# Kernel optimization log

Hardware: AMD Instinct MI355X
Metric: run time of the kernel (lower is better)

## Reference

```python
import jax, jax.numpy as jnp
import numpy as np

N_ATOMS = 65536
N_BONDS = 131072
N_MOLS = 512
D_IN = 16
D = 128
REPEAT = 3


def _dense(key, fan_in, fan_out):
    kw, kb = jax.random.split(key)
    scale = 1.0 / np.sqrt(fan_in)
    W = jax.random.normal(kw, (fan_in, fan_out), dtype=jnp.float32) * scale
    b = jnp.zeros((fan_out,), dtype=jnp.float32)
    return W, b


def setup_inputs() -> dict:
    key = jax.random.key(0)
    ks = jax.random.split(key, 12)
    atoms = jax.random.normal(ks[0], (N_ATOMS, D_IN), dtype=jnp.float32)
    bond_orders = jax.random.uniform(ks[1], (N_BONDS,), dtype=jnp.float32)
    bond_src = jax.random.randint(ks[2], (N_BONDS,), 0, N_ATOMS, dtype=jnp.int32)
    bond_dst = jax.random.randint(ks[3], (N_BONDS,), 0, N_ATOMS, dtype=jnp.int32)
    atom_mol = jnp.sort(jax.random.randint(ks[4], (N_ATOMS,), 0, N_MOLS, dtype=jnp.int32))
    bond_mol = jnp.sort(jax.random.randint(ks[5], (N_BONDS,), 0, N_MOLS, dtype=jnp.int32))
    W_fe, b_fe = _dense(ks[6], 1, D)      # f_e : bond order -> h_e
    W_fv, b_fv = _dense(ks[7], D_IN, D)   # f_v : atom feats -> h_v
    W_fu, b_fu = _dense(ks[8], D, D)      # f_u : per-mol init from aggregated nodes
    W_e, b_e = _dense(ks[9], 5 * D, D)    # phi_e(h_e, h_e0, h_left, h_right, u)
    W_v, b_v = _dense(ks[10], 4 * D, D)   # phi_v(h_v, h_v0, e_bar_i, u)
    W_u, b_u = _dense(ks[11], 4 * D, D)   # phi_u(h_u, h_u0, e_bar, v_bar)
    return dict(atoms=atoms, bond_orders=bond_orders, W_fe=W_fe, b_fe=b_fe,
                W_fv=W_fv, b_fv=b_fv, W_fu=W_fu, b_fu=b_fu, W_e=W_e, b_e=b_e,
                W_v=W_v, b_v=b_v, W_u=W_u, b_u=b_u,
                bond_src=bond_src, bond_dst=bond_dst,
                atom_mol=atom_mol, bond_mol=bond_mol)


def reference(atoms, bond_orders, W_fe, b_fe, W_fv, b_fv, W_fu, b_fu,
              W_e, b_e, W_v, b_v, W_u, b_u,
              bond_src, bond_dst, atom_mol, bond_mol):
    seg = lambda x, ids, n: jax.ops.segment_sum(x, ids, num_segments=n)
    relu = jax.nn.relu

    # f_e / f_v / f_u initial embeddings
    h_e0 = relu(bond_orders[:, None] @ W_fe + b_fe)           # [E, D]
    h_v0 = relu(atoms @ W_fv + b_fv)                          # [N, D]
    h_u0 = relu(seg(h_v0, atom_mol, N_MOLS) @ W_fu + b_fu)    # [M, D]

    h_e, h_v, h_u = h_e0, h_v0, h_u0
    for _ in range(REPEAT):
        # phi_e(e_k, e_k_0, v_rk, v_sk, u): gather endpoints and per-bond global
        h_left = h_v[bond_src]                                # [E, D]
        h_right = h_v[bond_dst]                               # [E, D]
        u_e = h_u[bond_mol]                                   # [E, D]
        h_e = relu(jnp.concatenate([h_e, h_e0, h_left, h_right, u_e], axis=1) @ W_e + b_e)
        # rho_e_v: sum of updated edges incident to each atom (one-hot mask == scatter-add)
        e_bar_i = seg(h_e, bond_src, N_ATOMS) + seg(h_e, bond_dst, N_ATOMS)  # [N, D]
        # phi_v(v_i, v_i_0, e_bar_i, u)
        h_v = relu(jnp.concatenate([h_v, h_v0, e_bar_i, h_u[atom_mol]], axis=1) @ W_v + b_v)
        # rho_e_u / rho_v_u: per-molecule segment sums
        e_bar = seg(h_e, bond_mol, N_MOLS)                    # [M, D]
        v_bar = seg(h_v, atom_mol, N_MOLS)                    # [M, D]
        # phi_u(u, u_0, e_bar, v_bar)
        h_u = relu(jnp.concatenate([h_u, h_u0, e_bar, v_bar], axis=1) @ W_u + b_u)
    return h_u
```

## Files before the change

kernel.cpp:

```cpp
#include <hip/hip_runtime.h>
#include <hip/hip_bf16.h>
#include <stdint.h>

#define N_ATOMS 65536
#define N_BONDS 131072
#define N_MOLS  512
#define D_IN    16
#define DD      128
#define REPEAT  3
#define PITCH   136

typedef __attribute__((ext_vector_type(8))) short s8b;
typedef __attribute__((ext_vector_type(4))) float f32x4;

__device__ __forceinline__ float us2f(unsigned short s) {
    unsigned int u = ((unsigned int)s) << 16;
    float f; __builtin_memcpy(&f, &u, 4); return f;
}
__device__ __forceinline__ unsigned short f2us(float f) {
    __hip_bfloat16 h = __float2bfloat16(f);
    unsigned short s; __builtin_memcpy(&s, &h, 2); return s;
}
__device__ __forceinline__ void acc8(float* a, uint4 v) {
    unsigned short w[8]; __builtin_memcpy(w, &v, 16);
#pragma unroll
    for (int j = 0; j < 8; j++) a[j] += us2f(w[j]);
}


__global__ void k_pack_w(const float* __restrict__ W, unsigned short* __restrict__ Wpk, int K) {
    int idx = blockIdx.x * 256 + threadIdx.x;
    if (idx >= K * 128) return;
    int k = idx >> 7, n = idx & 127;
    int c = k >> 7, ks = (k >> 5) & 3, quad = (k >> 3) & 3, j = k & 7;
    int pidx = (((c * 4 + ks) * 4 + quad) * 128 + n) * 8 + j;
    Wpk[pidx] = f2us(W[k * 128 + n]);
}

__global__ void k_deg(const int* __restrict__ bsrc, const int* __restrict__ bdst,
                      int* __restrict__ deg) {
    int e = blockIdx.x * 256 + threadIdx.x;
    atomicAdd(&deg[bsrc[e]], 1);
    atomicAdd(&deg[bdst[e]], 1);
}

__global__ void k_scan1(const int* __restrict__ deg, int* __restrict__ bsum) {
    __shared__ int red[256];
    int t = threadIdx.x;
    red[t] = deg[blockIdx.x * 256 + t];
    __syncthreads();
    for (int s = 128; s > 0; s >>= 1) {
        if (t < s) red[t] += red[t + s];
        __syncthreads();
    }
    if (t == 0) bsum[blockIdx.x] = red[0];
}

__global__ void k_scan2(const int* __restrict__ bsum, int* __restrict__ boff) {
    __shared__ int s[256];
    int t = threadIdx.x;
    s[t] = bsum[t];
    __syncthreads();
    if (t == 0) {
        int run = 0;
        for (int i = 0; i < 256; i++) { int v = s[i]; s[i] = run; run += v; }
    }
    __syncthreads();
    boff[t] = s[t];
}

__global__ void k_scan3(const int* __restrict__ deg, const int* __restrict__ boff,
                        int* __restrict__ rowptr, int* __restrict__ cursor) {
    __shared__ int s[256];
    int t = threadIdx.x;
    int i = blockIdx.x * 256 + t;
    int d = deg[i];
    s[t] = d;
    __syncthreads();
    for (int off = 1; off < 256; off <<= 1) {
        int v = (t >= off) ? s[t - off] : 0;
        __syncthreads();
        s[t] += v;
        __syncthreads();
    }
    int val = boff[blockIdx.x] + s[t] - d;
    rowptr[i] = val;
    cursor[i] = val;
    if (i == N_ATOMS - 1) rowptr[N_ATOMS] = val + d;
}

__global__ void k_fill(const int* __restrict__ bsrc, const int* __restrict__ bdst,
                       int* __restrict__ cursor, int* __restrict__ adj) {
    int e = blockIdx.x * 256 + threadIdx.x;
    int p = atomicAdd(&cursor[bsrc[e]], 1); adj[p] = e;
    int q = atomicAdd(&cursor[bdst[e]], 1); adj[q] = e;
}

__global__ void k_molptr2(const int* __restrict__ bmol, const int* __restrict__ amol,
                          int* __restrict__ bptr, int* __restrict__ aptr) {
    int m = threadIdx.x;
    if (m > N_MOLS) return;
    const int* ids = blockIdx.x ? amol : bmol;
    int rows = blockIdx.x ? N_ATOMS : N_BONDS;
    int* out = blockIdx.x ? aptr : bptr;
    int lo = 0, hi = rows;
    while (lo < hi) {
        int mid = (lo + hi) >> 1;
        if (ids[mid] < m) lo = mid + 1; else hi = mid;
    }
    out[m] = lo;
}


__global__ __launch_bounds__(256) void k_molsum_s(const unsigned short* __restrict__ x,
                                                  const int* __restrict__ mptr,
                                                  float* __restrict__ out, int S) {
    __shared__ float red[16 * 128];
    int m = blockIdx.x / S, s = blockIdx.x - m * S;
    int b = mptr[m], e = mptr[m + 1];
    int len = (e - b + S - 1) / S;
    int r0 = b + s * len;
    int r1 = min(r0 + len, e);
    int rl = threadIdx.x >> 4, g = threadIdx.x & 15;
    float acc[8] = {0,0,0,0,0,0,0,0};
    for (int r = r0 + rl; r < r1; r += 16)
        acc8(acc, *reinterpret_cast<const uint4*>(x + (size_t)r * DD + g * 8));
#pragma unroll
    for (int j = 0; j < 8; j++) red[rl * 128 + g * 8 + j] = acc[j];
    __syncthreads();
    if (threadIdx.x < 128) {
        int col = threadIdx.x;
        float sum = 0.f;
#pragma unroll
        for (int i = 0; i < 16; i++) sum += red[i * 128 + col];
        atomicAdd(&out[(size_t)m * DD + col], sum);
    }
}

__global__ void k_mol_init(const float* __restrict__ ns, const float* __restrict__ Wfu,
                           const float* __restrict__ bfu, float* __restrict__ hu0) {
    int idx = blockIdx.x * 256 + threadIdx.x;
    int m = idx >> 7, d = idx & 127;
    float acc = bfu[d];
    for (int k = 0; k < DD; k++)
        acc = fmaf(ns[m*DD + k], Wfu[k*DD + d], acc);
    hu0[idx] = fmaxf(acc, 0.f);
}

__global__ void k_yrow2(const float* __restrict__ hu,
                        const float* __restrict__ We, const float* __restrict__ be,
                        const float* __restrict__ Wv, const float* __restrict__ bv,
                        float* __restrict__ yue, float* __restrict__ yuv,
                        float* __restrict__ ebar, float* __restrict__ vbar) {
    int idx = blockIdx.x * 256 + threadIdx.x;
    if (idx < N_MOLS * DD) ebar[idx] = 0.f;
    else                   vbar[idx - N_MOLS * DD] = 0.f;
    int half = idx >= N_MOLS * DD;
    int md = half ? idx - N_MOLS * DD : idx;
    int m = md >> 7, d = md & 127;
    const float* W  = half ? Wv + 384 * DD : We + 512 * DD;
    float acc = half ? bv[d] : be[d];
    for (int k = 0; k < DD; k++)
        acc = fmaf(hu[m*DD + k], W[k*DD + d], acc);
    (half ? yuv : yue)[md] = acc;
}

__global__ __launch_bounds__(256) void k_ye0(
        const float* __restrict__ bo, const float* __restrict__ Wfe,
        const float* __restrict__ bfe, const unsigned short* __restrict__ Wpk,
        unsigned short* __restrict__ he, unsigned short* __restrict__ ye0) {
    __shared__ __align__(16) unsigned short xs[128 * PITCH];
    __shared__ float sbo[128];
    int tid = threadIdx.x;
    int e0 = blockIdx.x * 128;
    if (tid < 128) sbo[tid] = bo[e0 + tid];
    int wv = tid >> 6, lane = tid & 63, quad = lane >> 4, l15 = lane & 15;
    f32x4 acc[8][2];
#pragma unroll
    for (int mt = 0; mt < 8; mt++) {
        acc[mt][0] = (f32x4){0.f,0.f,0.f,0.f};
        acc[mt][1] = (f32x4){0.f,0.f,0.f,0.f};
    }
    __syncthreads();
    for (int t = 0; t < 8; t++) {
        int u = tid + t * 256;
        int i = u >> 4, g = (u & 15) * 8;
        float b = sbo[i];
        unsigned short tmp[8];
#pragma unroll
        for (int j = 0; j < 8; j++)
            tmp[j] = f2us(fmaxf(fmaf(b, Wfe[g + j], bfe[g + j]), 0.f));
        uint4 val; __builtin_memcpy(&val, tmp, 16);
        *reinterpret_cast<uint4*>(&xs[i * PITCH + g]) = val;
        *reinterpret_cast<uint4*>(he + (size_t)(e0 + i) * DD + g) = val;
    }
    __syncthreads();
#pragma unroll
    for (int ks = 0; ks < 4; ks++) {
        const unsigned short* wb = Wpk + ((1 * 4 + ks) * 4 + quad) * 1024 + (wv * 32 + l15) * 8;
        s8b b0 = *reinterpret_cast<const s8b*>(wb);
        s8b b1 = *reinterpret_cast<const s8b*>(wb + 128);
#pragma unroll
        for (int mt = 0; mt < 8; mt++) {
            s8b afr = *reinterpret_cast<const s8b*>(&xs[(mt*16 + l15) * PITCH + ks*32 + quad*8]);
            acc[mt][0] = __builtin_amdgcn_mfma_f32_16x16x32_bf16(afr, b0, acc[mt][0], 0, 0, 0);
            acc[mt][1] = __builtin_amdgcn_mfma_f32_16x16x32_bf16(afr, b1, acc[mt][1], 0, 0, 0);
        }
    }
#pragma unroll
    for (int mt = 0; mt < 8; mt++)
#pragma unroll
        for (int r = 0; r < 4; r++) {
            int row = e0 + mt*16 + quad*4 + r;
#pragma unroll
            for (int nt = 0; nt < 2; nt++) {
                int col = wv*32 + nt*16 + l15;
                ye0[(size_t)row * DD + col] = f2us(acc[mt][nt][r]);
            }
        }
}

__global__ __launch_bounds__(256) void k_nodes_f(
        const float* __restrict__ atoms, const float* __restrict__ Wfv,
        const float* __restrict__ bfv, const unsigned short* __restrict__ Wpk,
        unsigned short* __restrict__ hv, unsigned short* __restrict__ yv0,
        float* __restrict__ node_sum) {
    __shared__ __align__(16) unsigned short xs[128 * PITCH];
    int tid = threadIdx.x;
    int gid = blockIdx.x * 256 + tid;
    if (gid < N_MOLS * DD) node_sum[gid] = 0.f;
    int n0 = blockIdx.x * 128;
    int wv = tid >> 6, lane = tid & 63, quad = lane >> 4, l15 = lane & 15;
    f32x4 acc[8][2];
#pragma unroll
    for (int mt = 0; mt < 8; mt++) {
        acc[mt][0] = (f32x4){0.f,0.f,0.f,0.f};
        acc[mt][1] = (f32x4){0.f,0.f,0.f,0.f};
    }
    for (int t = 0; t < 8; t++) {
        int u = tid + t * 256;
        int i = u >> 4, g = (u & 15) * 8;
        int row = n0 + i;
        float a[D_IN];
#pragma unroll
        for (int k = 0; k < D_IN; k++) a[k] = atoms[(size_t)row * D_IN + k];
        unsigned short tmp[8];
#pragma unroll
        for (int j = 0; j < 8; j++) {
            float acc1 = bfv[g + j];
#pragma unroll
            for (int k = 0; k < D_IN; k++)
                acc1 = fmaf(a[k], Wfv[k*DD + g + j], acc1);
            tmp[j] = f2us(fmaxf(acc1, 0.f));
        }
        uint4 val; __builtin_memcpy(&val, tmp, 16);
        *reinterpret_cast<uint4*>(&xs[i * PITCH + g]) = val;
        *reinterpret_cast<uint4*>(hv + (size_t)row * DD + g) = val;
    }
    __syncthreads();
#pragma unroll
    for (int ks = 0; ks < 4; ks++) {
        const unsigned short* wb = Wpk + ((1 * 4 + ks) * 4 + quad) * 1024 + (wv * 32 + l15) * 8;
        s8b b0 = *reinterpret_cast<const s8b*>(wb);
        s8b b1 = *reinterpret_cast<const s8b*>(wb + 128);
#pragma unroll
        for (int mt = 0; mt < 8; mt++) {
            s8b afr = *reinterpret_cast<const s8b*>(&xs[(mt*16 + l15) * PITCH + ks*32 + quad*8]);
            acc[mt][0] = __builtin_amdgcn_mfma_f32_16x16x32_bf16(afr, b0, acc[mt][0], 0, 0, 0);
            acc[mt][1] = __builtin_amdgcn_mfma_f32_16x16x32_bf16(afr, b1, acc[mt][1], 0, 0, 0);
        }
    }
#pragma unroll
    for (int mt = 0; mt < 8; mt++)
#pragma unroll
        for (int r = 0; r < 4; r++) {
            int row = n0 + mt*16 + quad*4 + r;
#pragma unroll
            for (int nt = 0; nt < 2; nt++) {
                int col = wv*32 + nt*16 + l15;
                yv0[(size_t)row * DD + col] = f2us(acc[mt][nt][r]);
            }
        }
}

__global__ __launch_bounds__(256) void k_zsd(
        const unsigned short* __restrict__ hv, const unsigned short* __restrict__ Wpk,
        unsigned short* __restrict__ Zs, unsigned short* __restrict__ Zd) {
    __shared__ __align__(16) unsigned short xs[128 * PITCH];
    int tid = threadIdx.x;
    int n0 = blockIdx.x * 128;
    int wv = tid >> 6, lane = tid & 63, quad = lane >> 4, l15 = lane & 15;
    f32x4 aS[8][2], aD[8][2];
#pragma unroll
    for (int mt = 0; mt < 8; mt++) {
        aS[mt][0] = (f32x4){0.f,0.f,0.f,0.f}; aS[mt][1] = (f32x4){0.f,0.f,0.f,0.f};
        aD[mt][0] = (f32x4){0.f,0.f,0.f,0.f}; aD[mt][1] = (f32x4){0.f,0.f,0.f,0.f};
    }
    for (int t = 0; t < 8; t++) {
        int u = tid + t * 256;
        int i = u >> 4, g = (u & 15) * 8;
        *reinterpret_cast<uint4*>(&xs[i * PITCH + g]) =
            *reinterpret_cast<const uint4*>(hv + (size_t)(n0 + i) * DD + g);
    }
    __syncthreads();
#pragma unroll
    for (int ks = 0; ks < 4; ks++) {
        const unsigned short* wbS = Wpk + ((2 * 4 + ks) * 4 + quad) * 1024 + (wv * 32 + l15) * 8;
        const unsigned short* wbD = Wpk + ((3 * 4 + ks) * 4 + quad) * 1024 + (wv * 32 + l15) * 8;
        s8b s0 = *reinterpret_cast<const s8b*>(wbS);
        s8b s1 = *reinterpret_cast<const s8b*>(wbS + 128);
        s8b d0 = *reinterpret_cast<const s8b*>(wbD);
        s8b d1 = *reinterpret_cast<const s8b*>(wbD + 128);
#pragma unroll
        for (int mt = 0; mt < 8; mt++) {
            s8b afr = *reinterpret_cast<const s8b*>(&xs[(mt*16 + l15) * PITCH + ks*32 + quad*8]);
            aS[mt][0] = __builtin_amdgcn_mfma_f32_16x16x32_bf16(afr, s0, aS[mt][0], 0, 0, 0);
            aS[mt][1] = __builtin_amdgcn_mfma_f32_16x16x32_bf16(afr, s1, aS[mt][1], 0, 0, 0);
            aD[mt][0] = __builtin_amdgcn_mfma_f32_16x16x32_bf16(afr, d0, aD[mt][0], 0, 0, 0);
            aD[mt][1] = __builtin_amdgcn_mfma_f32_16x16x32_bf16(afr, d1, aD[mt][1], 0, 0, 0);
        }
    }
#pragma unroll
    for (int mt = 0; mt < 8; mt++)
#pragma unroll
        for (int r = 0; r < 4; r++) {
            int row = n0 + mt*16 + quad*4 + r;
#pragma unroll
            for (int nt = 0; nt < 2; nt++) {
                int col = wv*32 + nt*16 + l15;
                Zs[(size_t)row * DD + col] = f2us(aS[mt][nt][r]);
                Zd[(size_t)row * DD + col] = f2us(aD[mt][nt][r]);
            }
        }
}

__global__ __launch_bounds__(256) void k_phi_e(
        unsigned short* __restrict__ he, const unsigned short* __restrict__ ye0,
        const unsigned short* __restrict__ Zs, const unsigned short* __restrict__ Zd,
        const unsigned short* __restrict__ Wpk, const float* __restrict__ yue,
        const int* __restrict__ bsrc, const int* __restrict__ bdst,
        const int* __restrict__ bmol) {
    __shared__ __align__(16) unsigned short xs[128 * PITCH];
    __shared__ int ssrc[128], sdst[128], smol[128];
    int tid = threadIdx.x;
    int e0 = blockIdx.x * 128;
    if (tid < 128) {
        ssrc[tid] = bsrc[e0 + tid];
        sdst[tid] = bdst[e0 + tid];
        smol[tid] = bmol[e0 + tid];
    }
    int wv = tid >> 6, lane = tid & 63, quad = lane >> 4, l15 = lane & 15;
    f32x4 acc[8][2];
#pragma unroll
    for (int mt = 0; mt < 8; mt++) {
        acc[mt][0] = (f32x4){0.f,0.f,0.f,0.f};
        acc[mt][1] = (f32x4){0.f,0.f,0.f,0.f};
    }
    for (int t = 0; t < 8; t++) {
        int u = tid + t * 256;
        int i = u >> 4, g = (u & 15) * 8;
        *reinterpret_cast<uint4*>(&xs[i * PITCH + g]) =
            *reinterpret_cast<const uint4*>(he + (size_t)(e0 + i) * DD + g);
    }
    __syncthreads();
#pragma unroll
    for (int ks = 0; ks < 4; ks++) {
        const unsigned short* wb = Wpk + ((0 * 4 + ks) * 4 + quad) * 1024 + (wv * 32 + l15) * 8;
        s8b b0 = *reinterpret_cast<const s8b*>(wb);
        s8b b1 = *reinterpret_cast<const s8b*>(wb + 128);
#pragma unroll
        for (int mt = 0; mt < 8; mt++) {
            s8b afr = *reinterpret_cast<const s8b*>(&xs[(mt*16 + l15) * PITCH + ks*32 + quad*8]);
            acc[mt][0] = __builtin_amdgcn_mfma_f32_16x16x32_bf16(afr, b0, acc[mt][0], 0, 0, 0);
            acc[mt][1] = __builtin_amdgcn_mfma_f32_16x16x32_bf16(afr, b1, acc[mt][1], 0, 0, 0);
        }
    }
    __syncthreads();
    for (int t = 0; t < 8; t++) {
        int u = tid + t * 256;
        int i = u >> 4, g = (u & 15) * 8;
        float s[8] = {0,0,0,0,0,0,0,0};
        acc8(s, *reinterpret_cast<const uint4*>(ye0 + (size_t)(e0 + i) * DD + g));
        acc8(s, *reinterpret_cast<const uint4*>(Zs  + (size_t)ssrc[i] * DD + g));
        acc8(s, *reinterpret_cast<const uint4*>(Zd  + (size_t)sdst[i] * DD + g));
        const float* yr = yue + (size_t)smol[i] * DD + g;
        float4 y0 = *reinterpret_cast<const float4*>(yr);
        float4 y1 = *reinterpret_cast<const float4*>(yr + 4);
        s[0] += y0.x; s[1] += y0.y; s[2] += y0.z; s[3] += y0.w;
        s[4] += y1.x; s[5] += y1.y; s[6] += y1.z; s[7] += y1.w;
        unsigned short tmp[8];
#pragma unroll
        for (int j = 0; j < 8; j++) tmp[j] = f2us(s[j]);
        uint4 val; __builtin_memcpy(&val, tmp, 16);
        *reinterpret_cast<uint4*>(&xs[i * PITCH + g]) = val;
    }
    __syncthreads();
#pragma unroll
    for (int mt = 0; mt < 8; mt++)
#pragma unroll
        for (int r = 0; r < 4; r++) {
            int rl = mt*16 + quad*4 + r;
#pragma unroll
            for (int nt = 0; nt < 2; nt++) {
                int col = wv*32 + nt*16 + l15;
                float v = acc[mt][nt][r] + us2f(xs[rl * PITCH + col]);
                he[(size_t)(e0 + rl) * DD + col] = f2us(fmaxf(v, 0.f));
            }
        }
}

__global__ __launch_bounds__(256) void k_ebar(const unsigned short* __restrict__ he,
                                              const int* __restrict__ rowptr,
                                              const int* __restrict__ adj,
                                              unsigned short* __restrict__ ebar_i) {
    int n = blockIdx.x * 16 + (threadIdx.x >> 4);
    int g = threadIdx.x & 15;
    int b = rowptr[n], e = rowptr[n + 1];
    float acc[8] = {0,0,0,0,0,0,0,0};
    int j = b;
    for (; j + 3 < e; j += 4) {
        uint4 v0 = *reinterpret_cast<const uint4*>(he + (size_t)adj[j]     * DD + g * 8);
        uint4 v1 = *reinterpret_cast<const uint4*>(he + (size_t)adj[j + 1] * DD + g * 8);
        uint4 v2 = *reinterpret_cast<const uint4*>(he + (size_t)adj[j + 2] * DD + g * 8);
        uint4 v3 = *reinterpret_cast<const uint4*>(he + (size_t)adj[j + 3] * DD + g * 8);
        acc8(acc, v0); acc8(acc, v1); acc8(acc, v2); acc8(acc, v3);
    }
    for (; j < e; j++)
        acc8(acc, *reinterpret_cast<const uint4*>(he + (size_t)adj[j] * DD + g * 8));
    unsigned short o[8];
#pragma unroll
    for (int k = 0; k < 8; k++) o[k] = f2us(acc[k]);
    uint4 ov; __builtin_memcpy(&ov, o, 16);
    *reinterpret_cast<uint4*>(ebar_i + (size_t)n * DD + g * 8) = ov;
}

__global__ __launch_bounds__(256) void k_phi_v(
        unsigned short* __restrict__ hv, const unsigned short* __restrict__ ebar_i,
        const unsigned short* __restrict__ yv0,
        const unsigned short* __restrict__ Wpk, const float* __restrict__ yuv,
        const int* __restrict__ amol) {
    __shared__ __align__(16) unsigned short xs[128 * PITCH];
    __shared__ int smol[128];
    int tid = threadIdx.x;
    int n0 = blockIdx.x * 128;
    if (tid < 128) smol[tid] = amol[n0 + tid];
    int wv = tid >> 6, lane = tid & 63, quad = lane >> 4, l15 = lane & 15;
    f32x4 acc[8][2];
#pragma unroll
    for (int mt = 0; mt < 8; mt++) {
        acc[mt][0] = (f32x4){0.f,0.f,0.f,0.f};
        acc[mt][1] = (f32x4){0.f,0.f,0.f,0.f};
    }
    const unsigned short* bases[2] = { hv + (size_t)n0 * DD, ebar_i + (size_t)n0 * DD };
    const int wcs[2] = {0, 2};
    for (int c = 0; c < 2; c++) {
        if (c) __syncthreads();
        for (int t = 0; t < 8; t++) {
            int u = tid + t * 256;
            int i = u >> 4, g = (u & 15) * 8;
            *reinterpret_cast<uint4*>(&xs[i * PITCH + g]) =
                *reinterpret_cast<const uint4*>(bases[c] + (size_t)i * DD + g);
        }
        __syncthreads();
        int WC = wcs[c];
#pragma unroll
        for (int ks = 0; ks < 4; ks++) {
            const unsigned short* wb = Wpk + ((WC * 4 + ks) * 4 + quad) * 1024 + (wv * 32 + l15) * 8;
            s8b b0 = *reinterpret_cast<const s8b*>(wb);
            s8b b1 = *reinterpret_cast<const s8b*>(wb + 128);
#pragma unroll
            for (int mt = 0; mt < 8; mt++) {
                s8b afr = *reinterpret_cast<const s8b*>(&xs[(mt*16 + l15) * PITCH + ks*32 + quad*8]);
                acc[mt][0] = __builtin_amdgcn_mfma_f32_16x16x32_bf16(afr, b0, acc[mt][0], 0, 0, 0);
                acc[mt][1] = __builtin_amdgcn_mfma_f32_16x16x32_bf16(afr, b1, acc[mt][1], 0, 0, 0);
            }
        }
    }
    __syncthreads();
    for (int t = 0; t < 8; t++) {
        int u = tid + t * 256;
        int i = u >> 4, g = (u & 15) * 8;
        float s[8] = {0,0,0,0,0,0,0,0};
        acc8(s, *reinterpret_cast<const uint4*>(yv0 + (size_t)(n0 + i) * DD + g));
        const float* yr = yuv + (size_t)smol[i] * DD + g;
        float4 y0 = *reinterpret_cast<const float4*>(yr);
        float4 y1 = *reinterpret_cast<const float4*>(yr + 4);
        s[0] += y0.x; s[1] += y0.y; s[2] += y0.z; s[3] += y0.w;
        s[4] += y1.x; s[5] += y1.y; s[6] += y1.z; s[7] += y1.w;
        unsigned short tmp[8];
#pragma unroll
        for (int j = 0; j < 8; j++) tmp[j] = f2us(s[j]);
        uint4 val; __builtin_memcpy(&val, tmp, 16);
        *reinterpret_cast<uint4*>(&xs[i * PITCH + g]) = val;
    }
    __syncthreads();
#pragma unroll
    for (int mt = 0; mt < 8; mt++)
#pragma unroll
        for (int r = 0; r < 4; r++) {
            int rl = mt*16 + quad*4 + r;
#pragma unroll
            for (int nt = 0; nt < 2; nt++) {
                int col = wv*32 + nt*16 + l15;
                float v = acc[mt][nt][r] + us2f(xs[rl * PITCH + col]);
                hv[(size_t)(n0 + rl) * DD + col] = f2us(fmaxf(v, 0.f));
            }
        }
}

__global__ void k_phi_u(const float* __restrict__ hu_in, const float* __restrict__ hu0,
                        const float* __restrict__ ebar, const float* __restrict__ vbar,
                        const float* __restrict__ Wu, const float* __restrict__ bu,
                        float* __restrict__ hu_out, float* __restrict__ dout) {
    int idx = blockIdx.x * 256 + threadIdx.x;
    int m = idx >> 7, d = idx & 127;
    float acc = bu[d];
    const float* segs[4] = { hu_in + m*DD, hu0 + m*DD, ebar + m*DD, vbar + m*DD };
    for (int s = 0; s < 4; s++) {
        const float* x = segs[s];
        const float* W = Wu + (s*DD)*DD + d;
        for (int k = 0; k < DD; k++)
            acc = fmaf(x[k], W[k*DD], acc);
    }
    float v = fmaxf(acc, 0.f);
    hu_out[idx] = v;
    dout[idx] = v;
}


extern "C" void kernel_launch(void* const* d_in, const int* in_sizes, int n_in,
                              void* d_out, int out_size, void* d_ws, size_t ws_size,
                              hipStream_t stream) {
    const float* atoms = (const float*)d_in[0];
    const float* bo    = (const float*)d_in[1];
    const float* Wfe   = (const float*)d_in[2];
    const float* bfe   = (const float*)d_in[3];
    const float* Wfv   = (const float*)d_in[4];
    const float* bfv   = (const float*)d_in[5];
    const float* Wfu   = (const float*)d_in[6];
    const float* bfu   = (const float*)d_in[7];
    const float* We    = (const float*)d_in[8];
    const float* be    = (const float*)d_in[9];
    const float* Wv    = (const float*)d_in[10];
    const float* bv    = (const float*)d_in[11];
    const float* Wu    = (const float*)d_in[12];
    const float* bu    = (const float*)d_in[13];
    const int* bsrc    = (const int*)d_in[14];
    const int* bdst    = (const int*)d_in[15];
    const int* amol    = (const int*)d_in[16];
    const int* bmol    = (const int*)d_in[17];

    char* p = (char*)d_ws;
    auto alloc = [&](size_t bytes) {
        char* r = p;
        p += (bytes + 255) & ~(size_t)255;
        return r;
    };
    unsigned short* he     = (unsigned short*)alloc((size_t)N_BONDS * DD * 2);
    unsigned short* ye0    = (unsigned short*)alloc((size_t)N_BONDS * DD * 2);
    unsigned short* hv     = (unsigned short*)alloc((size_t)N_ATOMS * DD * 2);
    unsigned short* yv0    = (unsigned short*)alloc((size_t)N_ATOMS * DD * 2);
    unsigned short* Zs     = (unsigned short*)alloc((size_t)N_ATOMS * DD * 2);
    unsigned short* Zd     = (unsigned short*)alloc((size_t)N_ATOMS * DD * 2);
    unsigned short* ebar_i = (unsigned short*)alloc((size_t)N_ATOMS * DD * 2);
    unsigned short* WeP    = (unsigned short*)alloc((size_t)640 * DD * 2);
    unsigned short* WvP    = (unsigned short*)alloc((size_t)512 * DD * 2);
    int* deg      = (int*)alloc((size_t)N_ATOMS * 4);
    int* rowptr   = (int*)alloc((size_t)(N_ATOMS + 1) * 4);
    int* cursor   = (int*)alloc((size_t)N_ATOMS * 4);
    int* adj      = (int*)alloc((size_t)2 * N_BONDS * 4);
    int* bmol_ptr = (int*)alloc((size_t)(N_MOLS + 1) * 4);
    int* amol_ptr = (int*)alloc((size_t)(N_MOLS + 1) * 4);
    int* bsum     = (int*)alloc((size_t)256 * 4);
    int* boff     = (int*)alloc((size_t)256 * 4);
    float* node_sum = (float*)alloc((size_t)N_MOLS * DD * 4);
    float* hu0   = (float*)alloc((size_t)N_MOLS * DD * 4);
    float* huA   = (float*)alloc((size_t)N_MOLS * DD * 4);
    float* huB   = (float*)alloc((size_t)N_MOLS * DD * 4);
    float* ebar  = (float*)alloc((size_t)N_MOLS * DD * 4);
    float* vbar  = (float*)alloc((size_t)N_MOLS * DD * 4);
    float* yue   = (float*)alloc((size_t)N_MOLS * DD * 4);
    float* yuv   = (float*)alloc((size_t)N_MOLS * DD * 4);

    hipMemsetAsync(deg, 0, (size_t)N_ATOMS * 4, stream);
    k_deg<<<N_BONDS/256, 256, 0, stream>>>(bsrc, bdst, deg);
    k_scan1<<<256, 256, 0, stream>>>(deg, bsum);
    k_scan2<<<1, 256, 0, stream>>>(bsum, boff);
    k_scan3<<<256, 256, 0, stream>>>(deg, boff, rowptr, cursor);
    k_fill<<<N_BONDS/256, 256, 0, stream>>>(bsrc, bdst, cursor, adj);
    k_molptr2<<<2, 1024, 0, stream>>>(bmol, amol, bmol_ptr, amol_ptr);

    k_pack_w<<<(640*DD)/256, 256, 0, stream>>>(We, WeP, 640);
    k_pack_w<<<(512*DD)/256, 256, 0, stream>>>(Wv, WvP, 512);

    k_ye0<<<N_BONDS/128, 256, 0, stream>>>(bo, Wfe, bfe, WeP, he, ye0);
    k_nodes_f<<<N_ATOMS/128, 256, 0, stream>>>(atoms, Wfv, bfv, WvP, hv, yv0, node_sum);
    k_molsum_s<<<N_MOLS*2, 256, 0, stream>>>(hv, amol_ptr, node_sum, 2);
    k_mol_init<<<(N_MOLS*DD)/256, 256, 0, stream>>>(node_sum, Wfu, bfu, hu0);

    const float* hu_in = hu0; float* hu_out = huA;

    for (int r = 0; r < REPEAT; r++) {
        k_yrow2<<<(2*N_MOLS*DD)/256, 256, 0, stream>>>(hu_in, We, be, Wv, bv,
                                                       yue, yuv, ebar, vbar);
        k_zsd<<<N_ATOMS/128, 256, 0, stream>>>(hv, WeP, Zs, Zd);
        k_phi_e<<<N_BONDS/128, 256, 0, stream>>>(he, ye0, Zs, Zd, WeP, yue,
                                                 bsrc, bdst, bmol);
        k_ebar<<<N_ATOMS/16, 256, 0, stream>>>(he, rowptr, adj, ebar_i);
        k_molsum_s<<<N_MOLS*4, 256, 0, stream>>>(he, bmol_ptr, ebar, 4);
        k_phi_v<<<N_ATOMS/128, 256, 0, stream>>>(hv, ebar_i, yv0, WvP, yuv, amol);
        k_molsum_s<<<N_MOLS*2, 256, 0, stream>>>(hv, amol_ptr, vbar, 2);
        k_phi_u<<<(N_MOLS*DD)/256, 256, 0, stream>>>(hu_in, hu0, ebar, vbar, Wu, bu,
                                                     hu_out, (float*)d_out);

        hu_in = hu_out; hu_out = (hu_out == huA) ? huB : huA;
    }
}
```

Before: 523.2 us.

## Fuse per-molecule sums and edge gathers into GEMM epilogues, cut kernel launches

The per-molecule sums of edge and node features now happen inside the phi_e and phi_v epilogues. Each thread keeps a running sum over consecutive rows of the same molecule and flushes it with an atomicAdd, which replaces the separate k_molsum_s passes. The incident-edge gather (e_bar_i) moves into phi_v, so the ebar_i intermediate buffer and the k_ebar launch go away. The u-projection rows (yue/yuv) are computed in the mol_init and phi_u kernels, buffer zeroing moves into k_zsd, and the scan and weight-pack kernels are merged. This removes launches and extra global traffic, at the cost of more atomic contention and an irregular gather inside phi_v that may lower its occupancy.

```diff
diff --git a/kernel.cpp b/kernel.cpp
--- a/kernel.cpp
+++ b/kernel.cpp
@@ -28,13 +28,17 @@
 }
 
 
-__global__ void k_pack_w(const float* __restrict__ W, unsigned short* __restrict__ Wpk, int K) {
-    int idx = blockIdx.x * 256 + threadIdx.x;
-    if (idx >= K * 128) return;
+__device__ __forceinline__ void pack_one(const float* W, unsigned short* Wpk, int idx) {
     int k = idx >> 7, n = idx & 127;
     int c = k >> 7, ks = (k >> 5) & 3, quad = (k >> 3) & 3, j = k & 7;
-    int pidx = (((c * 4 + ks) * 4 + quad) * 128 + n) * 8 + j;
-    Wpk[pidx] = f2us(W[k * 128 + n]);
+    Wpk[(((c * 4 + ks) * 4 + quad) * 128 + n) * 8 + j] = f2us(W[k * 128 + n]);
+}
+__global__ void k_pack2(const float* __restrict__ We, const float* __restrict__ Wv,
+                        unsigned short* __restrict__ WeP, unsigned short* __restrict__ WvP) {
+    int idx = blockIdx.x * 256 + threadIdx.x;
+    const int NE = 640 * 128;
+    if (idx < NE) pack_one(We, WeP, idx);
+    else if (idx < NE + 512 * 128) pack_one(Wv, WvP, idx - NE);
 }
 
 __global__ void k_deg(const int* __restrict__ bsrc, const int* __restrict__ bdst,
@@ -56,23 +60,20 @@
     if (t == 0) bsum[blockIdx.x] = red[0];
 }
 
-__global__ void k_scan2(const int* __restrict__ bsum, int* __restrict__ boff) {
+__global__ void k_scan3b(const int* __restrict__ deg, const int* __restrict__ bsum,
+                         int* __restrict__ rowptr, int* __restrict__ cursor) {
+    __shared__ int sb[256];
     __shared__ int s[256];
     int t = threadIdx.x;
-    s[t] = bsum[t];
-    __syncthreads();
-    if (t == 0) {
-        int run = 0;
-        for (int i = 0; i < 256; i++) { int v = s[i]; s[i] = run; run += v; }
-    }
-    __syncthreads();
-    boff[t] = s[t];
-}
-
-__global__ void k_scan3(const int* __restrict__ deg, const int* __restrict__ boff,
-                        int* __restrict__ rowptr, int* __restrict__ cursor) {
-    __shared__ int s[256];
-    int t = threadIdx.x;
+    sb[t] = bsum[t];
+    __syncthreads();
+    for (int off = 1; off < 256; off <<= 1) {
+        int v = (t >= off) ? sb[t - off] : 0;
+        __syncthreads();
+        sb[t] += v;
+        __syncthreads();
+    }
+    int boff = sb[blockIdx.x] - bsum[blockIdx.x];
     int i = blockIdx.x * 256 + t;
     int d = deg[i];
     s[t] = d;
@@ -83,7 +84,7 @@
         s[t] += v;
         __syncthreads();
     }
-    int val = boff[blockIdx.x] + s[t] - d;
+    int val = boff + s[t] - d;
     rowptr[i] = val;
     cursor[i] = val;
     if (i == N_ATOMS - 1) rowptr[N_ATOMS] = val + d;
@@ -137,32 +138,31 @@
     }
 }
 
-__global__ void k_mol_init(const float* __restrict__ ns, const float* __restrict__ Wfu,
-                           const float* __restrict__ bfu, float* __restrict__ hu0) {
-    int idx = blockIdx.x * 256 + threadIdx.x;
-    int m = idx >> 7, d = idx & 127;
+__global__ __launch_bounds__(256) void k_mol_init_f(
+        const float* __restrict__ ns, const float* __restrict__ Wfu,
+        const float* __restrict__ bfu,
+        const float* __restrict__ We, const float* __restrict__ be,
+        const float* __restrict__ Wv, const float* __restrict__ bv,
+        float* __restrict__ hu0, float* __restrict__ yue, float* __restrict__ yuv) {
+    __shared__ float hrow[2 * DD];
+    int tid = threadIdx.x;
+    int ml = tid >> 7, d = tid & 127;
+    int m = blockIdx.x * 2 + ml;
     float acc = bfu[d];
     for (int k = 0; k < DD; k++)
         acc = fmaf(ns[m*DD + k], Wfu[k*DD + d], acc);
-    hu0[idx] = fmaxf(acc, 0.f);
-}
-
-__global__ void k_yrow2(const float* __restrict__ hu,
-                        const float* __restrict__ We, const float* __restrict__ be,
-                        const float* __restrict__ Wv, const float* __restrict__ bv,
-                        float* __restrict__ yue, float* __restrict__ yuv,
-                        float* __restrict__ ebar, float* __restrict__ vbar) {
-    int idx = blockIdx.x * 256 + threadIdx.x;
-    if (idx < N_MOLS * DD) ebar[idx] = 0.f;
-    else                   vbar[idx - N_MOLS * DD] = 0.f;
-    int half = idx >= N_MOLS * DD;
-    int md = half ? idx - N_MOLS * DD : idx;
-    int m = md >> 7, d = md & 127;
-    const float* W  = half ? Wv + 384 * DD : We + 512 * DD;
-    float acc = half ? bv[d] : be[d];
-    for (int k = 0; k < DD; k++)
-        acc = fmaf(hu[m*DD + k], W[k*DD + d], acc);
-    (half ? yuv : yue)[md] = acc;
+    float v = fmaxf(acc, 0.f);
+    hu0[m*DD + d] = v;
+    hrow[ml*DD + d] = v;
+    __syncthreads();
+    float ae = be[d], av = bv[d];
+    for (int k = 0; k < DD; k++) {
+        float h = hrow[ml*DD + k];
+        ae = fmaf(h, We[(512 + k)*DD + d], ae);
+        av = fmaf(h, Wv[(384 + k)*DD + d], av);
+    }
+    yue[m*DD + d] = ae;
+    yuv[m*DD + d] = av;
 }
 
 __global__ __launch_bounds__(256) void k_ye0(
@@ -285,9 +285,13 @@
 
 __global__ __launch_bounds__(256) void k_zsd(
         const unsigned short* __restrict__ hv, const unsigned short* __restrict__ Wpk,
-        unsigned short* __restrict__ Zs, unsigned short* __restrict__ Zd) {
+        unsigned short* __restrict__ Zs, unsigned short* __restrict__ Zd,
+        float* __restrict__ ebar, float* __restrict__ vbar) {
     __shared__ __align__(16) unsigned short xs[128 * PITCH];
     int tid = threadIdx.x;
+    int gid = blockIdx.x * 256 + tid;
+    if (gid < N_MOLS * DD) ebar[gid] = 0.f;
+    else                   vbar[gid - N_MOLS * DD] = 0.f;
     int n0 = blockIdx.x * 128;
     int wv = tid >> 6, lane = tid & 63, quad = lane >> 4, l15 = lane & 15;
     f32x4 aS[8][2], aD[8][2];
@@ -339,7 +343,7 @@
         const unsigned short* __restrict__ Zs, const unsigned short* __restrict__ Zd,
         const unsigned short* __restrict__ Wpk, const float* __restrict__ yue,
         const int* __restrict__ bsrc, const int* __restrict__ bdst,
-        const int* __restrict__ bmol) {
+        const int* __restrict__ bmol, float* __restrict__ ebar) {
     __shared__ __align__(16) unsigned short xs[128 * PITCH];
     __shared__ int ssrc[128], sdst[128], smol[128];
     int tid = threadIdx.x;
@@ -396,49 +400,31 @@
     }
     __syncthreads();
 #pragma unroll
-    for (int mt = 0; mt < 8; mt++)
-#pragma unroll
-        for (int r = 0; r < 4; r++) {
-            int rl = mt*16 + quad*4 + r;
-#pragma unroll
-            for (int nt = 0; nt < 2; nt++) {
-                int col = wv*32 + nt*16 + l15;
-                float v = acc[mt][nt][r] + us2f(xs[rl * PITCH + col]);
-                he[(size_t)(e0 + rl) * DD + col] = f2us(fmaxf(v, 0.f));
+    for (int nt = 0; nt < 2; nt++) {
+        int col = wv*32 + nt*16 + l15;
+        float run = 0.f;
+        int cur = smol[quad * 4];
+#pragma unroll
+        for (int mt = 0; mt < 8; mt++)
+#pragma unroll
+            for (int r = 0; r < 4; r++) {
+                int rl = mt*16 + quad*4 + r;
+                float v = fmaxf(acc[mt][nt][r] + us2f(xs[rl * PITCH + col]), 0.f);
+                he[(size_t)(e0 + rl) * DD + col] = f2us(v);
+                int m = smol[rl];
+                if (m != cur) { atomicAdd(&ebar[(size_t)cur * DD + col], run); run = 0.f; cur = m; }
+                run += v;
             }
-        }
-}
-
-__global__ __launch_bounds__(256) void k_ebar(const unsigned short* __restrict__ he,
-                                              const int* __restrict__ rowptr,
-                                              const int* __restrict__ adj,
-                                              unsigned short* __restrict__ ebar_i) {
-    int n = blockIdx.x * 16 + (threadIdx.x >> 4);
-    int g = threadIdx.x & 15;
-    int b = rowptr[n], e = rowptr[n + 1];
-    float acc[8] = {0,0,0,0,0,0,0,0};
-    int j = b;
-    for (; j + 3 < e; j += 4) {
-        uint4 v0 = *reinterpret_cast<const uint4*>(he + (size_t)adj[j]     * DD + g * 8);
-        uint4 v1 = *reinterpret_cast<const uint4*>(he + (size_t)adj[j + 1] * DD + g * 8);
-        uint4 v2 = *reinterpret_cast<const uint4*>(he + (size_t)adj[j + 2] * DD + g * 8);
-        uint4 v3 = *reinterpret_cast<const uint4*>(he + (size_t)adj[j + 3] * DD + g * 8);
-        acc8(acc, v0); acc8(acc, v1); acc8(acc, v2); acc8(acc, v3);
-    }
-    for (; j < e; j++)
-        acc8(acc, *reinterpret_cast<const uint4*>(he + (size_t)adj[j] * DD + g * 8));
-    unsigned short o[8];
-#pragma unroll
-    for (int k = 0; k < 8; k++) o[k] = f2us(acc[k]);
-    uint4 ov; __builtin_memcpy(&ov, o, 16);
-    *reinterpret_cast<uint4*>(ebar_i + (size_t)n * DD + g * 8) = ov;
+        atomicAdd(&ebar[(size_t)cur * DD + col], run);
+    }
 }
 
 __global__ __launch_bounds__(256) void k_phi_v(
-        unsigned short* __restrict__ hv, const unsigned short* __restrict__ ebar_i,
+        unsigned short* __restrict__ hv, const unsigned short* __restrict__ he,
+        const int* __restrict__ rowptr, const int* __restrict__ adj,
         const unsigned short* __restrict__ yv0,
         const unsigned short* __restrict__ Wpk, const float* __restrict__ yuv,
-        const int* __restrict__ amol) {
+        const int* __restrict__ amol, float* __restrict__ vbar) {
     __shared__ __align__(16) unsigned short xs[128 * PITCH];
     __shared__ int smol[128];
     int tid = threadIdx.x;
@@ -451,29 +437,60 @@
         acc[mt][0] = (f32x4){0.f,0.f,0.f,0.f};
         acc[mt][1] = (f32x4){0.f,0.f,0.f,0.f};
     }
-    const unsigned short* bases[2] = { hv + (size_t)n0 * DD, ebar_i + (size_t)n0 * DD };
-    const int wcs[2] = {0, 2};
-    for (int c = 0; c < 2; c++) {
-        if (c) __syncthreads();
-        for (int t = 0; t < 8; t++) {
-            int u = tid + t * 256;
-            int i = u >> 4, g = (u & 15) * 8;
-            *reinterpret_cast<uint4*>(&xs[i * PITCH + g]) =
-                *reinterpret_cast<const uint4*>(bases[c] + (size_t)i * DD + g);
-        }
-        __syncthreads();
-        int WC = wcs[c];
-#pragma unroll
-        for (int ks = 0; ks < 4; ks++) {
-            const unsigned short* wb = Wpk + ((WC * 4 + ks) * 4 + quad) * 1024 + (wv * 32 + l15) * 8;
-            s8b b0 = *reinterpret_cast<const s8b*>(wb);
-            s8b b1 = *reinterpret_cast<const s8b*>(wb + 128);
-#pragma unroll
-            for (int mt = 0; mt < 8; mt++) {
-                s8b afr = *reinterpret_cast<const s8b*>(&xs[(mt*16 + l15) * PITCH + ks*32 + quad*8]);
-                acc[mt][0] = __builtin_amdgcn_mfma_f32_16x16x32_bf16(afr, b0, acc[mt][0], 0, 0, 0);
-                acc[mt][1] = __builtin_amdgcn_mfma_f32_16x16x32_bf16(afr, b1, acc[mt][1], 0, 0, 0);
+    for (int t = 0; t < 8; t++) {
+        int u = tid + t * 256;
+        int i = u >> 4, g = (u & 15) * 8;
+        *reinterpret_cast<uint4*>(&xs[i * PITCH + g]) =
+            *reinterpret_cast<const uint4*>(hv + (size_t)(n0 + i) * DD + g);
+    }
+    __syncthreads();
+#pragma unroll
+    for (int ks = 0; ks < 4; ks++) {
+        const unsigned short* wb = Wpk + ((0 * 4 + ks) * 4 + quad) * 1024 + (wv * 32 + l15) * 8;
+        s8b b0 = *reinterpret_cast<const s8b*>(wb);
+        s8b b1 = *reinterpret_cast<const s8b*>(wb + 128);
+#pragma unroll
+        for (int mt = 0; mt < 8; mt++) {
+            s8b afr = *reinterpret_cast<const s8b*>(&xs[(mt*16 + l15) * PITCH + ks*32 + quad*8]);
+            acc[mt][0] = __builtin_amdgcn_mfma_f32_16x16x32_bf16(afr, b0, acc[mt][0], 0, 0, 0);
+            acc[mt][1] = __builtin_amdgcn_mfma_f32_16x16x32_bf16(afr, b1, acc[mt][1], 0, 0, 0);
+        }
+    }
+    __syncthreads();
+    {
+        int g = tid & 15, ab = tid >> 4;
+#pragma unroll
+        for (int k = 0; k < 8; k++) {
+            int a = ab + 16 * k;
+            int n = n0 + a;
+            int b = rowptr[n], e = rowptr[n + 1];
+            float s[8] = {0,0,0,0,0,0,0,0};
+            int j = b;
+            for (; j + 1 < e; j += 2) {
+                uint4 v0 = *reinterpret_cast<const uint4*>(he + (size_t)adj[j]     * DD + g * 8);
+                uint4 v1 = *reinterpret_cast<const uint4*>(he + (size_t)adj[j + 1] * DD + g * 8);
+                acc8(s, v0); acc8(s, v1);
             }
+            if (j < e)
+                acc8(s, *reinterpret_cast<const uint4*>(he + (size_t)adj[j] * DD + g * 8));
+            unsigned short tmp[8];
+#pragma unroll
+            for (int jj = 0; jj < 8; jj++) tmp[jj] = f2us(s[jj]);
+            uint4 val; __builtin_memcpy(&val, tmp, 16);
+            *reinterpret_cast<uint4*>(&xs[a * PITCH + g * 8]) = val;
+        }
+    }
+    __syncthreads();
+#pragma unroll
+    for (int ks = 0; ks < 4; ks++) {
+        const unsigned short* wb = Wpk + ((2 * 4 + ks) * 4 + quad) * 1024 + (wv * 32 + l15) * 8;
+        s8b b0 = *reinterpret_cast<const s8b*>(wb);
+        s8b b1 = *reinterpret_cast<const s8b*>(wb + 128);
+#pragma unroll
+        for (int mt = 0; mt < 8; mt++) {
+            s8b afr = *reinterpret_cast<const s8b*>(&xs[(mt*16 + l15) * PITCH + ks*32 + quad*8]);
+            acc[mt][0] = __builtin_amdgcn_mfma_f32_16x16x32_bf16(afr, b0, acc[mt][0], 0, 0, 0);
+            acc[mt][1] = __builtin_amdgcn_mfma_f32_16x16x32_bf16(afr, b1, acc[mt][1], 0, 0, 0);
         }
     }
     __syncthreads();
@@ -495,25 +512,37 @@
     }
     __syncthreads();
 #pragma unroll
-    for (int mt = 0; mt < 8; mt++)
-#pragma unroll
-        for (int r = 0; r < 4; r++) {
-            int rl = mt*16 + quad*4 + r;
-#pragma unroll
-            for (int nt = 0; nt < 2; nt++) {
-                int col = wv*32 + nt*16 + l15;
-                float v = acc[mt][nt][r] + us2f(xs[rl * PITCH + col]);
-                hv[(size_t)(n0 + rl) * DD + col] = f2us(fmaxf(v, 0.f));
+    for (int nt = 0; nt < 2; nt++) {
+        int col = wv*32 + nt*16 + l15;
+        float run = 0.f;
+        int cur = smol[quad * 4];
+#pragma unroll
+        for (int mt = 0; mt < 8; mt++)
+#pragma unroll
+            for (int r = 0; r < 4; r++) {
+                int rl = mt*16 + quad*4 + r;
+                float v = fmaxf(acc[mt][nt][r] + us2f(xs[rl * PITCH + col]), 0.f);
+                hv[(size_t)(n0 + rl) * DD + col] = f2us(v);
+                int m = smol[rl];
+                if (m != cur) { atomicAdd(&vbar[(size_t)cur * DD + col], run); run = 0.f; cur = m; }
+                run += v;
             }
-        }
-}
-
-__global__ void k_phi_u(const float* __restrict__ hu_in, const float* __restrict__ hu0,
-                        const float* __restrict__ ebar, const float* __restrict__ vbar,
-                        const float* __restrict__ Wu, const float* __restrict__ bu,
-                        float* __restrict__ hu_out, float* __restrict__ dout) {
-    int idx = blockIdx.x * 256 + threadIdx.x;
-    int m = idx >> 7, d = idx & 127;
+        atomicAdd(&vbar[(size_t)cur * DD + col], run);
+    }
+}
+
+__global__ __launch_bounds__(256) void k_phi_u_f(
+        const float* __restrict__ hu_in, const float* __restrict__ hu0,
+        const float* __restrict__ ebar, const float* __restrict__ vbar,
+        const float* __restrict__ Wu, const float* __restrict__ bu,
+        const float* __restrict__ We, const float* __restrict__ be,
+        const float* __restrict__ Wv, const float* __restrict__ bv,
+        float* __restrict__ hu_out, float* __restrict__ dout,
+        float* __restrict__ yue, float* __restrict__ yuv) {
+    __shared__ float hrow[2 * DD];
+    int tid = threadIdx.x;
+    int ml = tid >> 7, d = tid & 127;
+    int m = blockIdx.x * 2 + ml;
     float acc = bu[d];
     const float* segs[4] = { hu_in + m*DD, hu0 + m*DD, ebar + m*DD, vbar + m*DD };
     for (int s = 0; s < 4; s++) {
@@ -523,8 +552,18 @@
             acc = fmaf(x[k], W[k*DD], acc);
     }
     float v = fmaxf(acc, 0.f);
-    hu_out[idx] = v;
-    dout[idx] = v;
+    hu_out[m*DD + d] = v;
+    dout[m*DD + d] = v;
+    hrow[ml*DD + d] = v;
+    __syncthreads();
+    float ae = be[d], av = bv[d];
+    for (int k = 0; k < DD; k++) {
+        float h = hrow[ml*DD + k];
+        ae = fmaf(h, We[(512 + k)*DD + d], ae);
+        av = fmaf(h, Wv[(384 + k)*DD + d], av);
+    }
+    yue[m*DD + d] = ae;
+    yuv[m*DD + d] = av;
 }
 
 
@@ -562,7 +601,6 @@
     unsigned short* yv0    = (unsigned short*)alloc((size_t)N_ATOMS * DD * 2);
     unsigned short* Zs     = (unsigned short*)alloc((size_t)N_ATOMS * DD * 2);
     unsigned short* Zd     = (unsigned short*)alloc((size_t)N_ATOMS * DD * 2);
-    unsigned short* ebar_i = (unsigned short*)alloc((size_t)N_ATOMS * DD * 2);
     unsigned short* WeP    = (unsigned short*)alloc((size_t)640 * DD * 2);
     unsigned short* WvP    = (unsigned short*)alloc((size_t)512 * DD * 2);
     int* deg      = (int*)alloc((size_t)N_ATOMS * 4);
@@ -572,7 +610,6 @@
     int* bmol_ptr = (int*)alloc((size_t)(N_MOLS + 1) * 4);
     int* amol_ptr = (int*)alloc((size_t)(N_MOLS + 1) * 4);
     int* bsum     = (int*)alloc((size_t)256 * 4);
-    int* boff     = (int*)alloc((size_t)256 * 4);
     float* node_sum = (float*)alloc((size_t)N_MOLS * DD * 4);
     float* hu0   = (float*)alloc((size_t)N_MOLS * DD * 4);
     float* huA   = (float*)alloc((size_t)N_MOLS * DD * 4);
@@ -585,34 +622,29 @@
     hipMemsetAsync(deg, 0, (size_t)N_ATOMS * 4, stream);
     k_deg<<<N_BONDS/256, 256, 0, stream>>>(bsrc, bdst, deg);
     k_scan1<<<256, 256, 0, stream>>>(deg, bsum);
-    k_scan2<<<1, 256, 0, stream>>>(bsum, boff);
-    k_scan3<<<256, 256, 0, stream>>>(deg, boff, rowptr, cursor);
+    k_scan3b<<<256, 256, 0, stream>>>(deg, bsum, rowptr, cursor);
     k_fill<<<N_BONDS/256, 256, 0, stream>>>(bsrc, bdst, cursor, adj);
     k_molptr2<<<2, 1024, 0, stream>>>(bmol, amol, bmol_ptr, amol_ptr);
 
-    k_pack_w<<<(640*DD)/256, 256, 0, stream>>>(We, WeP, 640);
-    k_pack_w<<<(512*DD)/256, 256, 0, stream>>>(Wv, WvP, 512);
+    k_pack2<<<(640*DD + 512*DD)/256, 256, 0, stream>>>(We, Wv, WeP, WvP);
 
     k_ye0<<<N_BONDS/128, 256, 0, stream>>>(bo, Wfe, bfe, WeP, he, ye0);
     k_nodes_f<<<N_ATOMS/128, 256, 0, stream>>>(atoms, Wfv, bfv, WvP, hv, yv0, node_sum);
     k_molsum_s<<<N_MOLS*2, 256, 0, stream>>>(hv, amol_ptr, node_sum, 2);
-    k_mol_init<<<(N_MOLS*DD)/256, 256, 0, stream>>>(node_sum, Wfu, bfu, hu0);
+    k_mol_init_f<<<N_MOLS/2, 256, 0, stream>>>(node_sum, Wfu, bfu, We, be, Wv, bv,
+                                               hu0, yue, yuv);
 
     const float* hu_in = hu0; float* hu_out = huA;
 
     for (int r = 0; r < REPEAT; r++) {
-        k_yrow2<<<(2*N_MOLS*DD)/256, 256, 0, stream>>>(hu_in, We, be, Wv, bv,
-                                                       yue, yuv, ebar, vbar);
-        k_zsd<<<N_ATOMS/128, 256, 0, stream>>>(hv, WeP, Zs, Zd);
+        k_zsd<<<N_ATOMS/128, 256, 0, stream>>>(hv, WeP, Zs, Zd, ebar, vbar);
         k_phi_e<<<N_BONDS/128, 256, 0, stream>>>(he, ye0, Zs, Zd, WeP, yue,
-                                                 bsrc, bdst, bmol);
-        k_ebar<<<N_ATOMS/16, 256, 0, stream>>>(he, rowptr, adj, ebar_i);
-        k_molsum_s<<<N_MOLS*4, 256, 0, stream>>>(he, bmol_ptr, ebar, 4);
-        k_phi_v<<<N_ATOMS/128, 256, 0, stream>>>(hv, ebar_i, yv0, WvP, yuv, amol);
-        k_molsum_s<<<N_MOLS*2, 256, 0, stream>>>(hv, amol_ptr, vbar, 2);
-        k_phi_u<<<(N_MOLS*DD)/256, 256, 0, stream>>>(hu_in, hu0, ebar, vbar, Wu, bu,
-                                                     hu_out, (float*)d_out);
-
+                                                 bsrc, bdst, bmol, ebar);
+        k_phi_v<<<N_ATOMS/128, 256, 0, stream>>>(hv, he, rowptr, adj, yv0, WvP, yuv,
+                                                 amol, vbar);
+        k_phi_u_f<<<N_MOLS/2, 256, 0, stream>>>(hu_in, hu0, ebar, vbar, Wu, bu,
+                                                We, be, Wv, bv,
+                                                hu_out, (float*)d_out, yue, yuv);
         hu_in = hu_out; hu_out = (hu_out == huA) ? huB : huA;
     }
 }
```

New measurement: 537.7 us. +2.8%, slower.
